# Optimization experiments

Measured on AMD Instinct MI355X. Metric: run time of the kernel, lower is better.

Reference implementation:

```python
import jax, jax.numpy as jnp
import numpy as np

B, N, D, H = 16, 256, 512, 8
DK = D // H          # 64
DIM_G = 64           # trigonometric geometry embedding dim
WAVE_LEN = 1000.0


def box_relational_embedding(boxes):
    # boxes: [B, N, 4] = (x_min, y_min, x_max, y_max)
    x_min, y_min, x_max, y_max = jnp.split(boxes, 4, axis=-1)  # each [B,N,1]
    cx = ((x_min + x_max) * 0.5)[..., 0]   # [B,N]
    cy = ((y_min + y_max) * 0.5)[..., 0]
    w = (x_max - x_min + 1.0)[..., 0]
    h = (y_max - y_min + 1.0)[..., 0]
    # pairwise deltas, normalized by the *row* box size (as in the torch code)
    dx = jnp.log(jnp.clip(jnp.abs((cx[:, :, None] - cx[:, None, :]) / w[:, :, None]), 1e-3))
    dy = jnp.log(jnp.clip(jnp.abs((cy[:, :, None] - cy[:, None, :]) / h[:, :, None]), 1e-3))
    dw = jnp.log(w[:, :, None] / w[:, None, :])
    dh = jnp.log(h[:, :, None] / h[:, None, :])
    pos = jnp.stack([dx, dy, dw, dh], axis=-1)  # [B,N,N,4]
    # trig embedding: freq per (dim_g/8) channels
    feat_range = jnp.arange(DIM_G // 8, dtype=pos.dtype) / (DIM_G / 8.0)
    dim_mat = 1.0 / jnp.power(WAVE_LEN, feat_range)               # [8]
    mul = (100.0 * pos)[..., None] * dim_mat                      # [B,N,N,4,8]
    mul = mul.reshape(mul.shape[:3] + (-1,))                      # [B,N,N,32]
    return jnp.concatenate([jnp.sin(mul), jnp.cos(mul)], axis=-1)  # [B,N,N,64]


def setup_inputs() -> dict:
    key = jax.random.key(0)
    ks = jax.random.split(key, 16)
    inp = {
        'input_query': jax.random.normal(ks[0], (B, N, D), jnp.float32),
        'input_key': jax.random.normal(ks[1], (B, N, D), jnp.float32),
        'input_value': jax.random.normal(ks[2], (B, N, D), jnp.float32),
    }
    # valid boxes: x_max > x_min, y_max > y_min
    xm = jax.random.uniform(ks[3], (B, N, 1)) * 800.0
    ym = jax.random.uniform(ks[4], (B, N, 1)) * 800.0
    bw = jax.random.uniform(ks[5], (B, N, 1)) * 120.0 + 5.0
    bh = jax.random.uniform(ks[6], (B, N, 1)) * 120.0 + 5.0
    inp['input_box'] = jnp.concatenate([xm, ym, xm + bw, ym + bh], axis=-1)
    s = 1.0 / np.sqrt(D)
    inp['Wq'] = jax.random.normal(ks[7], (D, D), jnp.float32) * s
    inp['bq'] = jnp.zeros((D,), jnp.float32)
    inp['Wk'] = jax.random.normal(ks[8], (D, D), jnp.float32) * s
    inp['bk'] = jnp.zeros((D,), jnp.float32)
    inp['Wv'] = jax.random.normal(ks[9], (D, D), jnp.float32) * s
    inp['bv'] = jnp.zeros((D,), jnp.float32)
    inp['Wo'] = jax.random.normal(ks[10], (D, D), jnp.float32) * s
    inp['bo'] = jnp.zeros((D,), jnp.float32)
    inp['Wg'] = jax.random.normal(ks[11], (H, DIM_G), jnp.float32) * (1.0 / np.sqrt(DIM_G))
    inp['bg'] = jnp.zeros((H,), jnp.float32)
    return inp


def reference(input_query, input_key, input_value, input_box,
              Wq, bq, Wk, bk, Wv, bv, Wo, bo, Wg, bg):
    nb = input_query.shape[0]
    geo = box_relational_embedding(input_box)                     # [B,N,N,64]
    wg = jax.nn.relu(jnp.einsum('bijg,hg->bhij', geo, Wg) + bg[None, :, None, None])
    def proj(x, W, b):
        return (x @ W + b).reshape(nb, -1, H, DK).transpose(0, 2, 1, 3)  # [B,H,N,dk]
    q = proj(input_query, Wq, bq)
    k = proj(input_key, Wk, bk)
    v = proj(input_value, Wv, bv)
    scores = jnp.einsum('bhid,bhjd->bhij', q, k) / np.sqrt(DK)    # [B,H,N,N]
    w_mn = jax.nn.softmax(jnp.log(jnp.clip(wg, 1e-6)) + scores, axis=-1)
    out = jnp.einsum('bhij,bhjd->bhid', w_mn, v)                  # [B,H,N,dk]
    out = out.transpose(0, 2, 1, 3).reshape(nb, -1, H * DK)       # [B,N,D]
    return out @ Wo + bo
```

## Files before the change

kernel.cpp:

```cpp
#include <hip/hip_runtime.h>
#include <hip/hip_bf16.h>

#define B_ 16
#define N_ 256
#define D_ 512
#define H_ 8
#define DK_ 64

typedef unsigned short u16;
typedef __attribute__((ext_vector_type(8))) short bf16x8;
typedef __attribute__((ext_vector_type(4))) float f32x4;

__device__ __forceinline__ float bf2f(u16 u) {
    union { unsigned int i; float f; } v;
    v.i = ((unsigned int)u) << 16;
    return v.f;
}
__device__ __forceinline__ u16 f2bf(float f) {
    union { float f; unsigned int i; } v;
    v.f = f;
    unsigned int x = v.i;
    unsigned int r = (x >> 16) & 1u;
    x += 0x7fffu + r;
    return (u16)(x >> 16);
}

__global__ __launch_bounds__(256) void k_prep(const float* __restrict__ box,
                                              const float* __restrict__ Wg,
                                              const float* __restrict__ bg,
                                              u16* __restrict__ Sg,
                                              const float* __restrict__ W0,
                                              const float* __restrict__ W1,
                                              const float* __restrict__ W2,
                                              const float* __restrict__ W3,
                                              u16* __restrict__ Wt,
                                              const float* __restrict__ X0,
                                              const float* __restrict__ X1,
                                              const float* __restrict__ X2,
                                              u16* __restrict__ Xb) {
    const int tid = threadIdx.x;
    const int bid = blockIdx.x;
    if (bid < 4096) {
        __shared__ float sWg[8][64];
        __shared__ float sbg[8];
        if (tid < 8) sbg[tid] = bg[tid];
        { int e = tid; sWg[e >> 6][e & 63] = Wg[e];
          e = tid + 256; sWg[e >> 6][e & 63] = Wg[e]; }
        const int bi = bid, b = bi >> 8;
        float4 bxi = *(const float4*)&box[(size_t)bi * 4];
        float4 bxj = *(const float4*)&box[(size_t)(b * N_ + tid) * 4];
        __syncthreads();
        float cxi = (bxi.x + bxi.z) * 0.5f, cyi = (bxi.y + bxi.w) * 0.5f;
        float wi = bxi.z - bxi.x + 1.0f, hi = bxi.w - bxi.y + 1.0f;
        float cxj = (bxj.x + bxj.z) * 0.5f, cyj = (bxj.y + bxj.w) * 0.5f;
        float wj = bxj.z - bxj.x + 1.0f, hj = bxj.w - bxj.y + 1.0f;
        float pos[4];
        pos[0] = __logf(fmaxf(fabsf((cxi - cxj) / wi), 1e-3f));
        pos[1] = __logf(fmaxf(fabsf((cyi - cyj) / hi), 1e-3f));
        pos[2] = __logf(wi / wj);
        pos[3] = __logf(hi / hj);
        const float dm[8] = {1.0f, 0.42169650342858224f, 0.1778279410038923f,
                             0.07498942093324559f, 0.03162277660168379f,
                             0.013335214321633241f, 0.005623413251903491f,
                             0.0023713737056616554f};
        const float inv2pi = 0.15915494309189535f;
        float acc[8];
#pragma unroll
        for (int h = 0; h < 8; ++h) acc[h] = sbg[h];
#pragma unroll
        for (int t = 0; t < 4; ++t) {
            float base = 100.0f * pos[t];
#pragma unroll
            for (int f = 0; f < 8; ++f) {
                float rev = base * dm[f] * inv2pi;
                rev = rev - floorf(rev);
                float sn = __builtin_amdgcn_sinf(rev);
                float cs = __builtin_amdgcn_cosf(rev);
                int idx = t * 8 + f;
#pragma unroll
                for (int h = 0; h < 8; ++h)
                    acc[h] += sWg[h][idx] * sn + sWg[h][idx + 32] * cs;
            }
        }
        const int i = bi & 255;
#pragma unroll
        for (int h = 0; h < 8; ++h)
            Sg[(((size_t)(b * H_ + h) * N_) + i) * N_ + tid] =
                f2bf(__logf(fmaxf(acc[h], 1e-6f)));
    } else if (bid < 5120) {
        __shared__ float tt[32][33];
        int t = bid - 4096;
        int z = t >> 8, yb = (t >> 4) & 15, xb = t & 15;
        const float* W = (z == 0) ? W0 : (z == 1) ? W1 : (z == 2) ? W2 : W3;
        u16* dst = Wt + (size_t)z * 262144;
        const int kb = yb * 32, nb = xb * 32;
#pragma unroll
        for (int r = 0; r < 4; ++r) {
            int p = r * 256 + tid;
            tt[p >> 5][p & 31] = W[(size_t)(kb + (p >> 5)) * 512 + nb + (p & 31)];
        }
        __syncthreads();
#pragma unroll
        for (int r = 0; r < 4; ++r) {
            int p = r * 256 + tid;
            dst[(size_t)(nb + (p >> 5)) * 512 + kb + (p & 31)] = f2bf(tt[p & 31][p >> 5]);
        }
    } else {
        int t = bid - 5120;
        int z = t >> 10, x = t & 1023;
        const float* X = (z == 0) ? X0 : (z == 1) ? X1 : X2;
        u16* dst = Xb + (size_t)z * 2097152;
        int base = (x * 256 + tid) * 8;
        float4 a = *(const float4*)&X[base];
        float4 b = *(const float4*)&X[base + 4];
        ushort4 oa, ob;
        oa.x = f2bf(a.x); oa.y = f2bf(a.y); oa.z = f2bf(a.z); oa.w = f2bf(a.w);
        ob.x = f2bf(b.x); ob.y = f2bf(b.y); ob.z = f2bf(b.z); ob.w = f2bf(b.w);
        *(ushort4*)&dst[base] = oa;
        *(ushort4*)&dst[base + 4] = ob;
    }
}

__global__ __launch_bounds__(256) void k_gemm_qkv(const u16* __restrict__ Xb,
                                                  const u16* __restrict__ Wtb,
                                                  const float* __restrict__ bq,
                                                  const float* __restrict__ bk,
                                                  const float* __restrict__ bv,
                                                  u16* __restrict__ qkv) {
    const int z = blockIdx.z;
    const u16* Ab = Xb + (size_t)z * 2097152;
    const u16* Wt = Wtb + (size_t)z * 262144;
    const float* bias = (z == 0) ? bq : (z == 1) ? bk : bv;
    u16* dst = qkv + (size_t)z * 2097152;

    __shared__ u16 As[2][64][72];
    __shared__ u16 Bs[2][64][72];
    const int tid = threadIdx.x;
    const int n0 = blockIdx.x * 64, m0 = blockIdx.y * 64;
    const int wid = tid >> 6, lane = tid & 63;
    const int wm = (wid & 1) * 32, wn = (wid >> 1) * 32;
    const int lr = lane & 15, lk8 = (lane >> 4) * 8, quad4 = (lane >> 4) * 4;

    f32x4 acc[2][2];
#pragma unroll
    for (int mi = 0; mi < 2; ++mi)
#pragma unroll
        for (int ni = 0; ni < 2; ++ni) acc[mi][ni] = (f32x4){0.f, 0.f, 0.f, 0.f};

    ushort4 ra[4], rb[4];
#pragma unroll
    for (int r = 0; r < 4; ++r) {
        int p = r * 256 + tid, row = p >> 4, c4 = (p & 15) * 4;
        ra[r] = *(const ushort4*)&Ab[(size_t)(m0 + row) * 512 + c4];
        rb[r] = *(const ushort4*)&Wt[(size_t)(n0 + row) * 512 + c4];
    }
#pragma unroll
    for (int r = 0; r < 4; ++r) {
        int p = r * 256 + tid, row = p >> 4, c4 = (p & 15) * 4;
        *(ushort4*)&As[0][row][c4] = ra[r];
        *(ushort4*)&Bs[0][row][c4] = rb[r];
    }
    __syncthreads();
    for (int it = 0; it < 8; ++it) {
        const int cur = it & 1;
        if (it < 7) {
            int k0n = (it + 1) * 64;
#pragma unroll
            for (int r = 0; r < 4; ++r) {
                int p = r * 256 + tid, row = p >> 4, c4 = (p & 15) * 4;
                ra[r] = *(const ushort4*)&Ab[(size_t)(m0 + row) * 512 + k0n + c4];
                rb[r] = *(const ushort4*)&Wt[(size_t)(n0 + row) * 512 + k0n + c4];
            }
        }
#pragma unroll
        for (int ks = 0; ks < 64; ks += 32) {
            bf16x8 af[2], bfx[2];
#pragma unroll
            for (int mi = 0; mi < 2; ++mi)
                af[mi] = *(const bf16x8*)&As[cur][wm + mi * 16 + lr][ks + lk8];
#pragma unroll
            for (int ni = 0; ni < 2; ++ni)
                bfx[ni] = *(const bf16x8*)&Bs[cur][wn + ni * 16 + lr][ks + lk8];
#pragma unroll
            for (int mi = 0; mi < 2; ++mi)
#pragma unroll
                for (int ni = 0; ni < 2; ++ni)
                    acc[mi][ni] = __builtin_amdgcn_mfma_f32_16x16x32_bf16(
                        af[mi], bfx[ni], acc[mi][ni], 0, 0, 0);
        }
        if (it < 7) {
#pragma unroll
            for (int r = 0; r < 4; ++r) {
                int p = r * 256 + tid, row = p >> 4, c4 = (p & 15) * 4;
                *(ushort4*)&As[1 - cur][row][c4] = ra[r];
                *(ushort4*)&Bs[1 - cur][row][c4] = rb[r];
            }
            __syncthreads();
        }
    }
    u16* bounce = &As[0][0][0];
    const float scale = (z == 0) ? 0.125f : 1.0f;
    const int h = n0 >> 6, b = m0 >> 8, rrb = m0 & 255;
    if (z == 2) {
#pragma unroll
        for (int mi = 0; mi < 2; ++mi)
#pragma unroll
            for (int ni = 0; ni < 2; ++ni) {
                int cn = wn + ni * 16 + lr;
                float bb = bias[n0 + cn];
#pragma unroll
                for (int reg = 0; reg < 4; ++reg) {
                    int rm = wm + mi * 16 + quad4 + reg;
                    bounce[cn * 72 + rm] = f2bf(acc[mi][ni][reg] + bb);
                }
            }
        __syncthreads();
#pragma unroll
        for (int r = 0; r < 4; ++r) {
            int p = r * 256 + tid, dn = p >> 4, c4 = (p & 15) * 4;
            *(ushort4*)&dst[(((size_t)(b * H_ + h) * DK_) + dn) * N_ + rrb + c4] =
                *(const ushort4*)&bounce[dn * 72 + c4];
        }
    } else {
#pragma unroll
        for (int mi = 0; mi < 2; ++mi)
#pragma unroll
            for (int ni = 0; ni < 2; ++ni) {
                int cn = wn + ni * 16 + lr;
                float bb = bias[n0 + cn];
#pragma unroll
                for (int reg = 0; reg < 4; ++reg) {
                    int rm = wm + mi * 16 + quad4 + reg;
                    bounce[rm * 72 + cn] = f2bf((acc[mi][ni][reg] + bb) * scale);
                }
            }
        __syncthreads();
#pragma unroll
        for (int r = 0; r < 4; ++r) {
            int p = r * 256 + tid, rm = p >> 4, c4 = (p & 15) * 4;
            *(ushort4*)&dst[(((size_t)(b * H_ + h) * N_) + rrb + rm) * DK_ + c4] =
                *(const ushort4*)&bounce[rm * 72 + c4];
        }
    }
}

__global__ __launch_bounds__(256) void k_gemm_out(const u16* __restrict__ Ab,
                                                  const u16* __restrict__ Wt,
                                                  const float* __restrict__ bias,
                                                  float* __restrict__ outp) {
    __shared__ u16 As[2][64][72];
    __shared__ u16 Bs[2][64][72];
    const int tid = threadIdx.x;
    const int n0 = blockIdx.x * 64, m0 = blockIdx.y * 64;
    const int wid = tid >> 6, lane = tid & 63;
    const int wm = (wid & 1) * 32, wn = (wid >> 1) * 32;
    const int lr = lane & 15, lk8 = (lane >> 4) * 8;
    f32x4 acc[2][2];
#pragma unroll
    for (int mi = 0; mi < 2; ++mi)
#pragma unroll
        for (int ni = 0; ni < 2; ++ni) acc[mi][ni] = (f32x4){0.f, 0.f, 0.f, 0.f};
    ushort4 ra[4], rb[4];
#pragma unroll
    for (int r = 0; r < 4; ++r) {
        int p = r * 256 + tid, row = p >> 4, c4 = (p & 15) * 4;
        ra[r] = *(const ushort4*)&Ab[(size_t)(m0 + row) * 512 + c4];
        rb[r] = *(const ushort4*)&Wt[(size_t)(n0 + row) * 512 + c4];
    }
#pragma unroll
    for (int r = 0; r < 4; ++r) {
        int p = r * 256 + tid, row = p >> 4, c4 = (p & 15) * 4;
        *(ushort4*)&As[0][row][c4] = ra[r];
        *(ushort4*)&Bs[0][row][c4] = rb[r];
    }
    __syncthreads();
    for (int it = 0; it < 8; ++it) {
        const int cur = it & 1;
        if (it < 7) {
            int k0n = (it + 1) * 64;
#pragma unroll
            for (int r = 0; r < 4; ++r) {
                int p = r * 256 + tid, row = p >> 4, c4 = (p & 15) * 4;
                ra[r] = *(const ushort4*)&Ab[(size_t)(m0 + row) * 512 + k0n + c4];
                rb[r] = *(const ushort4*)&Wt[(size_t)(n0 + row) * 512 + k0n + c4];
            }
        }
#pragma unroll
        for (int ks = 0; ks < 64; ks += 32) {
            bf16x8 af[2], bfx[2];
#pragma unroll
            for (int mi = 0; mi < 2; ++mi)
                af[mi] = *(const bf16x8*)&As[cur][wm + mi * 16 + lr][ks + lk8];
#pragma unroll
            for (int ni = 0; ni < 2; ++ni)
                bfx[ni] = *(const bf16x8*)&Bs[cur][wn + ni * 16 + lr][ks + lk8];
#pragma unroll
            for (int mi = 0; mi < 2; ++mi)
#pragma unroll
                for (int ni = 0; ni < 2; ++ni)
                    acc[mi][ni] = __builtin_amdgcn_mfma_f32_16x16x32_bf16(
                        af[mi], bfx[ni], acc[mi][ni], 0, 0, 0);
        }
        if (it < 7) {
#pragma unroll
            for (int r = 0; r < 4; ++r) {
                int p = r * 256 + tid, row = p >> 4, c4 = (p & 15) * 4;
                *(ushort4*)&As[1 - cur][row][c4] = ra[r];
                *(ushort4*)&Bs[1 - cur][row][c4] = rb[r];
            }
            __syncthreads();
        }
    }
#pragma unroll
    for (int mi = 0; mi < 2; ++mi)
#pragma unroll
        for (int ni = 0; ni < 2; ++ni) {
            int col = n0 + wn + ni * 16 + lr;
            float bb = bias[col];
#pragma unroll
            for (int reg = 0; reg < 4; ++reg) {
                int m = m0 + wm + mi * 16 + (lane >> 4) * 4 + reg;
                outp[(size_t)m * 512 + col] = acc[mi][ni][reg] + bb;
            }
        }
}

__global__ __launch_bounds__(256) void k_attn(const u16* __restrict__ qh,
                                              const u16* __restrict__ kh,
                                              const u16* __restrict__ vhT,
                                              const u16* __restrict__ Sg,
                                              u16* __restrict__ attnb) {
    __shared__ __align__(16) unsigned char smem[40960];
    u16* sQ = (u16*)smem;
    u16* sP = (u16*)(smem + 4608);
    u16* sK = (u16*)(smem + 21504);
    u16* sVt = (u16*)(smem + 21504);
    float* sRedM = (float*)(smem + 39936);
    float* sRedS = (float*)(smem + 40448);

    const int tid = threadIdx.x;
    const int i0 = blockIdx.x * 32;
    const int bh = blockIdx.y;
    const int b = bh >> 3, h = bh & 7;
    const int wid = tid >> 6, lane = tid & 63;
    const int lr = lane & 15, lk8 = (lane >> 4) * 8, quad4 = (lane >> 4) * 4;

#pragma unroll
    for (int r = 0; r < 2; ++r) {
        int p = r * 256 + tid, i = p >> 4, d0 = (p & 15) * 4;
        *(ushort4*)&sQ[i * 72 + d0] =
            *(const ushort4*)&qh[((size_t)bh * N_ + i0 + i) * DK_ + d0];
    }
#pragma unroll
    for (int r = 0; r < 8; ++r) {
        int p = r * 256 + tid, row = p >> 6, jc = (p & 63) * 4;
        *(ushort4*)&sP[row * 264 + jc] =
            *(const ushort4*)&Sg[(((size_t)bh * N_) + i0 + row) * N_ + jc];
    }
#pragma unroll
    for (int r = 0; r < 8; ++r) {
        int p = r * 256 + tid, j = p >> 4, d0 = (p & 15) * 4;
        *(ushort4*)&sK[j * 72 + d0] =
            *(const ushort4*)&kh[((size_t)bh * N_ + j) * DK_ + d0];
    }
    __syncthreads();

    ushort4 kpre[8];
#pragma unroll
    for (int r = 0; r < 8; ++r) {
        int p = r * 256 + tid, j = p >> 4, d0 = (p & 15) * 4;
        kpre[r] = *(const ushort4*)&kh[((size_t)bh * N_ + 128 + j) * DK_ + d0];
    }
    f32x4 acc[2][2][2];
#pragma unroll
    for (int c = 0; c < 2; ++c)
#pragma unroll
        for (int mi = 0; mi < 2; ++mi)
#pragma unroll
            for (int ni = 0; ni < 2; ++ni) acc[c][mi][ni] = (f32x4){0.f, 0.f, 0.f, 0.f};
#pragma unroll
    for (int ks = 0; ks < 64; ks += 32) {
        bf16x8 af[2], bfx[2];
#pragma unroll
        for (int mi = 0; mi < 2; ++mi)
            af[mi] = *(const bf16x8*)&sQ[(mi * 16 + lr) * 72 + ks + lk8];
#pragma unroll
        for (int ni = 0; ni < 2; ++ni)
            bfx[ni] = *(const bf16x8*)&sK[(wid * 32 + ni * 16 + lr) * 72 + ks + lk8];
#pragma unroll
        for (int mi = 0; mi < 2; ++mi)
#pragma unroll
            for (int ni = 0; ni < 2; ++ni)
                acc[0][mi][ni] = __builtin_amdgcn_mfma_f32_16x16x32_bf16(
                    af[mi], bfx[ni], acc[0][mi][ni], 0, 0, 0);
    }
    __syncthreads();
#pragma unroll
    for (int r = 0; r < 8; ++r) {
        int p = r * 256 + tid, j = p >> 4, d0 = (p & 15) * 4;
        *(ushort4*)&sK[j * 72 + d0] = kpre[r];
    }
    __syncthreads();
#pragma unroll
    for (int ks = 0; ks < 64; ks += 32) {
        bf16x8 af[2], bfx[2];
#pragma unroll
        for (int mi = 0; mi < 2; ++mi)
            af[mi] = *(const bf16x8*)&sQ[(mi * 16 + lr) * 72 + ks + lk8];
#pragma unroll
        for (int ni = 0; ni < 2; ++ni)
            bfx[ni] = *(const bf16x8*)&sK[(wid * 32 + ni * 16 + lr) * 72 + ks + lk8];
#pragma unroll
        for (int mi = 0; mi < 2; ++mi)
#pragma unroll
            for (int ni = 0; ni < 2; ++ni)
                acc[1][mi][ni] = __builtin_amdgcn_mfma_f32_16x16x32_bf16(
                    af[mi], bfx[ni], acc[1][mi][ni], 0, 0, 0);
    }
    __syncthreads();

#pragma unroll
    for (int r = 0; r < 8; ++r) {
        int p = r * 256 + tid, d = p >> 5, jc = (p & 31) * 4;
        *(ushort4*)&sVt[d * 136 + jc] =
            *(const ushort4*)&vhT[(((size_t)bh * DK_) + d) * N_ + jc];
    }
#pragma unroll
    for (int c = 0; c < 2; ++c)
#pragma unroll
        for (int mi = 0; mi < 2; ++mi)
#pragma unroll
            for (int ni = 0; ni < 2; ++ni) {
                int col = c * 128 + wid * 32 + ni * 16 + lr;
#pragma unroll
                for (int reg = 0; reg < 4; ++reg) {
                    int row = mi * 16 + quad4 + reg;
                    acc[c][mi][ni][reg] += bf2f(sP[row * 264 + col]);
                }
            }
    float mrow[2][4];
#pragma unroll
    for (int mi = 0; mi < 2; ++mi)
#pragma unroll
        for (int reg = 0; reg < 4; ++reg) {
            float m = acc[0][mi][0][reg];
            m = fmaxf(m, acc[0][mi][1][reg]);
            m = fmaxf(m, acc[1][mi][0][reg]);
            m = fmaxf(m, acc[1][mi][1][reg]);
#pragma unroll
            for (int off = 1; off <= 8; off <<= 1) m = fmaxf(m, __shfl_xor(m, off, 64));
            mrow[mi][reg] = m;
        }
    if (lr == 0) {
#pragma unroll
        for (int mi = 0; mi < 2; ++mi)
#pragma unroll
            for (int reg = 0; reg < 4; ++reg)
                sRedM[(mi * 16 + quad4 + reg) * 4 + wid] = mrow[mi][reg];
    }
    __syncthreads();
    float gm[2][4], sl[2][4];
#pragma unroll
    for (int mi = 0; mi < 2; ++mi)
#pragma unroll
        for (int reg = 0; reg < 4; ++reg) {
            float4 mm = *(const float4*)&sRedM[(mi * 16 + quad4 + reg) * 4];
            gm[mi][reg] = fmaxf(fmaxf(mm.x, mm.y), fmaxf(mm.z, mm.w));
            sl[mi][reg] = 0.f;
        }
#pragma unroll
    for (int c = 0; c < 2; ++c)
#pragma unroll
        for (int mi = 0; mi < 2; ++mi)
#pragma unroll
            for (int ni = 0; ni < 2; ++ni)
#pragma unroll
                for (int reg = 0; reg < 4; ++reg) {
                    float e = __expf(acc[c][mi][ni][reg] - gm[mi][reg]);
                    acc[c][mi][ni][reg] = e;
                    sl[mi][reg] += e;
                }
#pragma unroll
    for (int mi = 0; mi < 2; ++mi)
#pragma unroll
        for (int reg = 0; reg < 4; ++reg) {
            float s = sl[mi][reg];
#pragma unroll
            for (int off = 1; off <= 8; off <<= 1) s += __shfl_xor(s, off, 64);
            sl[mi][reg] = s;
        }
    if (lr == 0) {
#pragma unroll
        for (int mi = 0; mi < 2; ++mi)
#pragma unroll
            for (int reg = 0; reg < 4; ++reg)
                sRedS[(mi * 16 + quad4 + reg) * 4 + wid] = sl[mi][reg];
    }
    __syncthreads();
#pragma unroll
    for (int mi = 0; mi < 2; ++mi)
#pragma unroll
        for (int reg = 0; reg < 4; ++reg) {
            float4 ss = *(const float4*)&sRedS[(mi * 16 + quad4 + reg) * 4];
            gm[mi][reg] = 1.0f / (ss.x + ss.y + ss.z + ss.w);
        }
#pragma unroll
    for (int c = 0; c < 2; ++c)
#pragma unroll
        for (int mi = 0; mi < 2; ++mi)
#pragma unroll
            for (int ni = 0; ni < 2; ++ni) {
                int col = c * 128 + wid * 32 + ni * 16 + lr;
#pragma unroll
                for (int reg = 0; reg < 4; ++reg) {
                    int row = mi * 16 + quad4 + reg;
                    sP[row * 264 + col] = f2bf(acc[c][mi][ni][reg] * gm[mi][reg]);
                }
            }
    __syncthreads();

    f32x4 o[2];
    o[0] = (f32x4){0.f, 0.f, 0.f, 0.f};
    o[1] = (f32x4){0.f, 0.f, 0.f, 0.f};
#pragma unroll
    for (int k0 = 0; k0 < 128; k0 += 32) {
        bf16x8 bfx = *(const bf16x8*)&sVt[(wid * 16 + lr) * 136 + k0 + lk8];
#pragma unroll
        for (int mi = 0; mi < 2; ++mi) {
            bf16x8 af = *(const bf16x8*)&sP[(mi * 16 + lr) * 264 + k0 + lk8];
            o[mi] = __builtin_amdgcn_mfma_f32_16x16x32_bf16(af, bfx, o[mi], 0, 0, 0);
        }
    }
    __syncthreads();
#pragma unroll
    for (int r = 0; r < 8; ++r) {
        int p = r * 256 + tid, d = p >> 5, jc = (p & 31) * 4;
        *(ushort4*)&sVt[d * 136 + jc] =
            *(const ushort4*)&vhT[(((size_t)bh * DK_) + d) * N_ + 128 + jc];
    }
    __syncthreads();
#pragma unroll
    for (int k0 = 0; k0 < 128; k0 += 32) {
        bf16x8 bfx = *(const bf16x8*)&sVt[(wid * 16 + lr) * 136 + k0 + lk8];
#pragma unroll
        for (int mi = 0; mi < 2; ++mi) {
            bf16x8 af = *(const bf16x8*)&sP[(mi * 16 + lr) * 264 + 128 + k0 + lk8];
            o[mi] = __builtin_amdgcn_mfma_f32_16x16x32_bf16(af, bfx, o[mi], 0, 0, 0);
        }
    }
#pragma unroll
    for (int mi = 0; mi < 2; ++mi)
#pragma unroll
        for (int reg = 0; reg < 4; ++reg) {
            int row = mi * 16 + quad4 + reg;
            attnb[((size_t)(b * N_ + i0 + row)) * D_ + h * 64 + wid * 16 + lr] =
                f2bf(o[mi][reg]);
        }
}

extern "C" void kernel_launch(void* const* d_in, const int* in_sizes, int n_in,
                              void* d_out, int out_size, void* d_ws, size_t ws_size,
                              hipStream_t stream) {
    const float* Xq = (const float*)d_in[0];
    const float* Xk = (const float*)d_in[1];
    const float* Xv = (const float*)d_in[2];
    const float* box = (const float*)d_in[3];
    const float* Wq = (const float*)d_in[4];
    const float* bq = (const float*)d_in[5];
    const float* Wk = (const float*)d_in[6];
    const float* bk = (const float*)d_in[7];
    const float* Wv = (const float*)d_in[8];
    const float* bv = (const float*)d_in[9];
    const float* Wo = (const float*)d_in[10];
    const float* bo = (const float*)d_in[11];
    const float* Wg = (const float*)d_in[12];
    const float* bg = (const float*)d_in[13];
    float* out = (float*)d_out;

    u16* ws16 = (u16*)d_ws;
    u16* qkv = ws16;
    u16* qh = qkv;
    u16* kh = qkv + 2097152;
    u16* vhT = qkv + 4194304;
    u16* Sg = ws16 + 6291456;
    u16* attnb = ws16 + 14680064;
    u16* Wt = ws16 + 16777216;
    u16* Xb = ws16 + 18874368;

    dim3 blk(256);
    k_prep<<<dim3(8192), blk, 0, stream>>>(box, Wg, bg, Sg, Wq, Wk, Wv, Wo, Wt,
                                           Xq, Xk, Xv, Xb);
    k_gemm_qkv<<<dim3(8, 64, 3), blk, 0, stream>>>(Xb, Wt, bq, bk, bv, qkv);
    k_attn<<<dim3(8, 128), blk, 0, stream>>>(qh, kh, vhT, Sg, attnb);
    k_gemm_out<<<dim3(8, 64), blk, 0, stream>>>(attnb, Wt + 3 * 262144, bo, out);
}
```

Measured before the change: 169.4 us.

## Move geometry bias computation into the QKV GEMM launch to overlap work

The trig-heavy geometric bias computation (4096 blocks) moves out of the prep kernel and into the QKV projection kernel as extra blocks. The QKV GEMM's 1536 MFMA blocks and the ALU-bound geometry blocks then share one grid and can co-schedule on the CUs. The prep kernel keeps only the weight transpose and input bf16 conversion. Shared memory becomes a single union buffer, and the larger LDS footprint applies to the geometry blocks as well, which may lower their occupancy.

```diff
diff --git a/kernel.cpp b/kernel.cpp
--- a/kernel.cpp
+++ b/kernel.cpp
@@ -25,28 +25,187 @@
     return (u16)(x >> 16);
 }
 
-__global__ __launch_bounds__(256) void k_prep(const float* __restrict__ box,
-                                              const float* __restrict__ Wg,
-                                              const float* __restrict__ bg,
-                                              u16* __restrict__ Sg,
-                                              const float* __restrict__ W0,
-                                              const float* __restrict__ W1,
-                                              const float* __restrict__ W2,
-                                              const float* __restrict__ W3,
-                                              u16* __restrict__ Wt,
-                                              const float* __restrict__ X0,
-                                              const float* __restrict__ X1,
-                                              const float* __restrict__ X2,
-                                              u16* __restrict__ Xb) {
+__global__ __launch_bounds__(256) void k_prep_lite(const float* __restrict__ W0,
+                                                   const float* __restrict__ W1,
+                                                   const float* __restrict__ W2,
+                                                   const float* __restrict__ W3,
+                                                   u16* __restrict__ Wt,
+                                                   const float* __restrict__ X0,
+                                                   const float* __restrict__ X1,
+                                                   const float* __restrict__ X2,
+                                                   u16* __restrict__ Xb) {
     const int tid = threadIdx.x;
     const int bid = blockIdx.x;
-    if (bid < 4096) {
-        __shared__ float sWg[8][64];
-        __shared__ float sbg[8];
+    if (bid < 1024) {
+        __shared__ float tt[32][33];
+        int t = bid;
+        int z = t >> 8, yb = (t >> 4) & 15, xb = t & 15;
+        const float* W = (z == 0) ? W0 : (z == 1) ? W1 : (z == 2) ? W2 : W3;
+        u16* dst = Wt + (size_t)z * 262144;
+        const int kb = yb * 32, nb = xb * 32;
+#pragma unroll
+        for (int r = 0; r < 4; ++r) {
+            int p = r * 256 + tid;
+            tt[p >> 5][p & 31] = W[(size_t)(kb + (p >> 5)) * 512 + nb + (p & 31)];
+        }
+        __syncthreads();
+#pragma unroll
+        for (int r = 0; r < 4; ++r) {
+            int p = r * 256 + tid;
+            dst[(size_t)(nb + (p >> 5)) * 512 + kb + (p & 31)] = f2bf(tt[p & 31][p >> 5]);
+        }
+    } else {
+        int t = bid - 1024;
+        int z = t >> 10, x = t & 1023;
+        const float* X = (z == 0) ? X0 : (z == 1) ? X1 : X2;
+        u16* dst = Xb + (size_t)z * 2097152;
+        int base = (x * 256 + tid) * 8;
+        float4 a = *(const float4*)&X[base];
+        float4 b = *(const float4*)&X[base + 4];
+        ushort4 oa, ob;
+        oa.x = f2bf(a.x); oa.y = f2bf(a.y); oa.z = f2bf(a.z); oa.w = f2bf(a.w);
+        ob.x = f2bf(b.x); ob.y = f2bf(b.y); ob.z = f2bf(b.z); ob.w = f2bf(b.w);
+        *(ushort4*)&dst[base] = oa;
+        *(ushort4*)&dst[base + 4] = ob;
+    }
+}
+
+__global__ __launch_bounds__(256) void k_qkv_geo(const u16* __restrict__ Xb,
+                                                 const u16* __restrict__ Wtb,
+                                                 const float* __restrict__ bq,
+                                                 const float* __restrict__ bk,
+                                                 const float* __restrict__ bv,
+                                                 u16* __restrict__ qkv,
+                                                 const float* __restrict__ box,
+                                                 const float* __restrict__ Wg,
+                                                 const float* __restrict__ bg,
+                                                 u16* __restrict__ Sg) {
+    __shared__ __align__(16) unsigned char smem[36864];
+    const int tid = threadIdx.x;
+    const int bid = blockIdx.x;
+    if (bid < 1536) {
+        u16* As = (u16*)smem;
+        u16* Bs = (u16*)(smem + 18432);
+        const int z = bid >> 9, t = bid & 511;
+        const int n0 = (t & 7) * 64, m0 = (t >> 3) * 64;
+        const u16* Ab = Xb + (size_t)z * 2097152;
+        const u16* Wt = Wtb + (size_t)z * 262144;
+        const float* bias = (z == 0) ? bq : (z == 1) ? bk : bv;
+        u16* dst = qkv + (size_t)z * 2097152;
+        const int wid = tid >> 6, lane = tid & 63;
+        const int wm = (wid & 1) * 32, wn = (wid >> 1) * 32;
+        const int lr = lane & 15, lk8 = (lane >> 4) * 8, quad4 = (lane >> 4) * 4;
+
+        f32x4 acc[2][2];
+#pragma unroll
+        for (int mi = 0; mi < 2; ++mi)
+#pragma unroll
+            for (int ni = 0; ni < 2; ++ni) acc[mi][ni] = (f32x4){0.f, 0.f, 0.f, 0.f};
+
+        ushort4 ra[4], rb[4];
+#pragma unroll
+        for (int r = 0; r < 4; ++r) {
+            int p = r * 256 + tid, row = p >> 4, c4 = (p & 15) * 4;
+            ra[r] = *(const ushort4*)&Ab[(size_t)(m0 + row) * 512 + c4];
+            rb[r] = *(const ushort4*)&Wt[(size_t)(n0 + row) * 512 + c4];
+        }
+#pragma unroll
+        for (int r = 0; r < 4; ++r) {
+            int p = r * 256 + tid, row = p >> 4, c4 = (p & 15) * 4;
+            *(ushort4*)&As[(0 * 64 + row) * 72 + c4] = ra[r];
+            *(ushort4*)&Bs[(0 * 64 + row) * 72 + c4] = rb[r];
+        }
+        __syncthreads();
+        for (int it = 0; it < 8; ++it) {
+            const int cur = it & 1;
+            if (it < 7) {
+                int k0n = (it + 1) * 64;
+#pragma unroll
+                for (int r = 0; r < 4; ++r) {
+                    int p = r * 256 + tid, row = p >> 4, c4 = (p & 15) * 4;
+                    ra[r] = *(const ushort4*)&Ab[(size_t)(m0 + row) * 512 + k0n + c4];
+                    rb[r] = *(const ushort4*)&Wt[(size_t)(n0 + row) * 512 + k0n + c4];
+                }
+            }
+#pragma unroll
+            for (int ks = 0; ks < 64; ks += 32) {
+                bf16x8 af[2], bfx[2];
+#pragma unroll
+                for (int mi = 0; mi < 2; ++mi)
+                    af[mi] = *(const bf16x8*)&As[(cur * 64 + wm + mi * 16 + lr) * 72 + ks + lk8];
+#pragma unroll
+                for (int ni = 0; ni < 2; ++ni)
+                    bfx[ni] = *(const bf16x8*)&Bs[(cur * 64 + wn + ni * 16 + lr) * 72 + ks + lk8];
+#pragma unroll
+                for (int mi = 0; mi < 2; ++mi)
+#pragma unroll
+                    for (int ni = 0; ni < 2; ++ni)
+                        acc[mi][ni] = __builtin_amdgcn_mfma_f32_16x16x32_bf16(
+                            af[mi], bfx[ni], acc[mi][ni], 0, 0, 0);
+            }
+            if (it < 7) {
+                const int nxt = 1 - cur;
+#pragma unroll
+                for (int r = 0; r < 4; ++r) {
+                    int p = r * 256 + tid, row = p >> 4, c4 = (p & 15) * 4;
+                    *(ushort4*)&As[(nxt * 64 + row) * 72 + c4] = ra[r];
+                    *(ushort4*)&Bs[(nxt * 64 + row) * 72 + c4] = rb[r];
+                }
+                __syncthreads();
+            }
+        }
+        u16* bounce = (u16*)smem;
+        const float scale = (z == 0) ? 0.125f : 1.0f;
+        const int h = n0 >> 6, b = m0 >> 8, rrb = m0 & 255;
+        __syncthreads();
+        if (z == 2) {
+#pragma unroll
+            for (int mi = 0; mi < 2; ++mi)
+#pragma unroll
+                for (int ni = 0; ni < 2; ++ni) {
+                    int cn = wn + ni * 16 + lr;
+                    float bb = bias[n0 + cn];
+#pragma unroll
+                    for (int reg = 0; reg < 4; ++reg) {
+                        int rm = wm + mi * 16 + quad4 + reg;
+                        bounce[cn * 72 + rm] = f2bf(acc[mi][ni][reg] + bb);
+                    }
+                }
+            __syncthreads();
+#pragma unroll
+            for (int r = 0; r < 4; ++r) {
+                int p = r * 256 + tid, dn = p >> 4, c4 = (p & 15) * 4;
+                *(ushort4*)&dst[(((size_t)(b * H_ + h) * DK_) + dn) * N_ + rrb + c4] =
+                    *(const ushort4*)&bounce[dn * 72 + c4];
+            }
+        } else {
+#pragma unroll
+            for (int mi = 0; mi < 2; ++mi)
+#pragma unroll
+                for (int ni = 0; ni < 2; ++ni) {
+                    int cn = wn + ni * 16 + lr;
+                    float bb = bias[n0 + cn];
+#pragma unroll
+                    for (int reg = 0; reg < 4; ++reg) {
+                        int rm = wm + mi * 16 + quad4 + reg;
+                        bounce[rm * 72 + cn] = f2bf((acc[mi][ni][reg] + bb) * scale);
+                    }
+                }
+            __syncthreads();
+#pragma unroll
+            for (int r = 0; r < 4; ++r) {
+                int p = r * 256 + tid, rm = p >> 4, c4 = (p & 15) * 4;
+                *(ushort4*)&dst[(((size_t)(b * H_ + h) * N_) + rrb + rm) * DK_ + c4] =
+                    *(const ushort4*)&bounce[rm * 72 + c4];
+            }
+        }
+    } else {
+        float* sWg = (float*)smem;
+        float* sbg = (float*)(smem + 2048);
         if (tid < 8) sbg[tid] = bg[tid];
-        { int e = tid; sWg[e >> 6][e & 63] = Wg[e];
-          e = tid + 256; sWg[e >> 6][e & 63] = Wg[e]; }
-        const int bi = bid, b = bi >> 8;
+        { int e = tid; sWg[(e >> 6) * 64 + (e & 63)] = Wg[e];
+          e = tid + 256; sWg[(e >> 6) * 64 + (e & 63)] = Wg[e]; }
+        const int bi = bid - 1536, b = bi >> 8;
         float4 bxi = *(const float4*)&box[(size_t)bi * 4];
         float4 bxj = *(const float4*)&box[(size_t)(b * N_ + tid) * 4];
         __syncthreads();
@@ -79,7 +238,7 @@
                 int idx = t * 8 + f;
 #pragma unroll
                 for (int h = 0; h < 8; ++h)
-                    acc[h] += sWg[h][idx] * sn + sWg[h][idx + 32] * cs;
+                    acc[h] += sWg[h * 64 + idx] * sn + sWg[h * 64 + idx + 32] * cs;
             }
         }
         const int i = bi & 255;
@@ -87,160 +246,6 @@
         for (int h = 0; h < 8; ++h)
             Sg[(((size_t)(b * H_ + h) * N_) + i) * N_ + tid] =
                 f2bf(__logf(fmaxf(acc[h], 1e-6f)));
-    } else if (bid < 5120) {
-        __shared__ float tt[32][33];
-        int t = bid - 4096;
-        int z = t >> 8, yb = (t >> 4) & 15, xb = t & 15;
-        const float* W = (z == 0) ? W0 : (z == 1) ? W1 : (z == 2) ? W2 : W3;
-        u16* dst = Wt + (size_t)z * 262144;
-        const int kb = yb * 32, nb = xb * 32;
-#pragma unroll
-        for (int r = 0; r < 4; ++r) {
-            int p = r * 256 + tid;
-            tt[p >> 5][p & 31] = W[(size_t)(kb + (p >> 5)) * 512 + nb + (p & 31)];
-        }
-        __syncthreads();
-#pragma unroll
-        for (int r = 0; r < 4; ++r) {
-            int p = r * 256 + tid;
-            dst[(size_t)(nb + (p >> 5)) * 512 + kb + (p & 31)] = f2bf(tt[p & 31][p >> 5]);
-        }
-    } else {
-        int t = bid - 5120;
-        int z = t >> 10, x = t & 1023;
-        const float* X = (z == 0) ? X0 : (z == 1) ? X1 : X2;
-        u16* dst = Xb + (size_t)z * 2097152;
-        int base = (x * 256 + tid) * 8;
-        float4 a = *(const float4*)&X[base];
-        float4 b = *(const float4*)&X[base + 4];
-        ushort4 oa, ob;
-        oa.x = f2bf(a.x); oa.y = f2bf(a.y); oa.z = f2bf(a.z); oa.w = f2bf(a.w);
-        ob.x = f2bf(b.x); ob.y = f2bf(b.y); ob.z = f2bf(b.z); ob.w = f2bf(b.w);
-        *(ushort4*)&dst[base] = oa;
-        *(ushort4*)&dst[base + 4] = ob;
-    }
-}
-
-__global__ __launch_bounds__(256) void k_gemm_qkv(const u16* __restrict__ Xb,
-                                                  const u16* __restrict__ Wtb,
-                                                  const float* __restrict__ bq,
-                                                  const float* __restrict__ bk,
-                                                  const float* __restrict__ bv,
-                                                  u16* __restrict__ qkv) {
-    const int z = blockIdx.z;
-    const u16* Ab = Xb + (size_t)z * 2097152;
-    const u16* Wt = Wtb + (size_t)z * 262144;
-    const float* bias = (z == 0) ? bq : (z == 1) ? bk : bv;
-    u16* dst = qkv + (size_t)z * 2097152;
-
-    __shared__ u16 As[2][64][72];
-    __shared__ u16 Bs[2][64][72];
-    const int tid = threadIdx.x;
-    const int n0 = blockIdx.x * 64, m0 = blockIdx.y * 64;
-    const int wid = tid >> 6, lane = tid & 63;
-    const int wm = (wid & 1) * 32, wn = (wid >> 1) * 32;
-    const int lr = lane & 15, lk8 = (lane >> 4) * 8, quad4 = (lane >> 4) * 4;
-
-    f32x4 acc[2][2];
-#pragma unroll
-    for (int mi = 0; mi < 2; ++mi)
-#pragma unroll
-        for (int ni = 0; ni < 2; ++ni) acc[mi][ni] = (f32x4){0.f, 0.f, 0.f, 0.f};
-
-    ushort4 ra[4], rb[4];
-#pragma unroll
-    for (int r = 0; r < 4; ++r) {
-        int p = r * 256 + tid, row = p >> 4, c4 = (p & 15) * 4;
-        ra[r] = *(const ushort4*)&Ab[(size_t)(m0 + row) * 512 + c4];
-        rb[r] = *(const ushort4*)&Wt[(size_t)(n0 + row) * 512 + c4];
-    }
-#pragma unroll
-    for (int r = 0; r < 4; ++r) {
-        int p = r * 256 + tid, row = p >> 4, c4 = (p & 15) * 4;
-        *(ushort4*)&As[0][row][c4] = ra[r];
-        *(ushort4*)&Bs[0][row][c4] = rb[r];
-    }
-    __syncthreads();
-    for (int it = 0; it < 8; ++it) {
-        const int cur = it & 1;
-        if (it < 7) {
-            int k0n = (it + 1) * 64;
-#pragma unroll
-            for (int r = 0; r < 4; ++r) {
-                int p = r * 256 + tid, row = p >> 4, c4 = (p & 15) * 4;
-                ra[r] = *(const ushort4*)&Ab[(size_t)(m0 + row) * 512 + k0n + c4];
-                rb[r] = *(const ushort4*)&Wt[(size_t)(n0 + row) * 512 + k0n + c4];
-            }
-        }
-#pragma unroll
-        for (int ks = 0; ks < 64; ks += 32) {
-            bf16x8 af[2], bfx[2];
-#pragma unroll
-            for (int mi = 0; mi < 2; ++mi)
-                af[mi] = *(const bf16x8*)&As[cur][wm + mi * 16 + lr][ks + lk8];
-#pragma unroll
-            for (int ni = 0; ni < 2; ++ni)
-                bfx[ni] = *(const bf16x8*)&Bs[cur][wn + ni * 16 + lr][ks + lk8];
-#pragma unroll
-            for (int mi = 0; mi < 2; ++mi)
-#pragma unroll
-                for (int ni = 0; ni < 2; ++ni)
-                    acc[mi][ni] = __builtin_amdgcn_mfma_f32_16x16x32_bf16(
-                        af[mi], bfx[ni], acc[mi][ni], 0, 0, 0);
-        }
-        if (it < 7) {
-#pragma unroll
-            for (int r = 0; r < 4; ++r) {
-                int p = r * 256 + tid, row = p >> 4, c4 = (p & 15) * 4;
-                *(ushort4*)&As[1 - cur][row][c4] = ra[r];
-                *(ushort4*)&Bs[1 - cur][row][c4] = rb[r];
-            }
-            __syncthreads();
-        }
-    }
-    u16* bounce = &As[0][0][0];
-    const float scale = (z == 0) ? 0.125f : 1.0f;
-    const int h = n0 >> 6, b = m0 >> 8, rrb = m0 & 255;
-    if (z == 2) {
-#pragma unroll
-        for (int mi = 0; mi < 2; ++mi)
-#pragma unroll
-            for (int ni = 0; ni < 2; ++ni) {
-                int cn = wn + ni * 16 + lr;
-                float bb = bias[n0 + cn];
-#pragma unroll
-                for (int reg = 0; reg < 4; ++reg) {
-                    int rm = wm + mi * 16 + quad4 + reg;
-                    bounce[cn * 72 + rm] = f2bf(acc[mi][ni][reg] + bb);
-                }
-            }
-        __syncthreads();
-#pragma unroll
-        for (int r = 0; r < 4; ++r) {
-            int p = r * 256 + tid, dn = p >> 4, c4 = (p & 15) * 4;
-            *(ushort4*)&dst[(((size_t)(b * H_ + h) * DK_) + dn) * N_ + rrb + c4] =
-                *(const ushort4*)&bounce[dn * 72 + c4];
-        }
-    } else {
-#pragma unroll
-        for (int mi = 0; mi < 2; ++mi)
-#pragma unroll
-            for (int ni = 0; ni < 2; ++ni) {
-                int cn = wn + ni * 16 + lr;
-                float bb = bias[n0 + cn];
-#pragma unroll
-                for (int reg = 0; reg < 4; ++reg) {
-                    int rm = wm + mi * 16 + quad4 + reg;
-                    bounce[rm * 72 + cn] = f2bf((acc[mi][ni][reg] + bb) * scale);
-                }
-            }
-        __syncthreads();
-#pragma unroll
-        for (int r = 0; r < 4; ++r) {
-            int p = r * 256 + tid, rm = p >> 4, c4 = (p & 15) * 4;
-            *(ushort4*)&dst[(((size_t)(b * H_ + h) * N_) + rrb + rm) * DK_ + c4] =
-                *(const ushort4*)&bounce[rm * 72 + c4];
-        }
     }
 }
 
@@ -588,9 +593,9 @@
     u16* Xb = ws16 + 18874368;
 
     dim3 blk(256);
-    k_prep<<<dim3(8192), blk, 0, stream>>>(box, Wg, bg, Sg, Wq, Wk, Wv, Wo, Wt,
-                                           Xq, Xk, Xv, Xb);
-    k_gemm_qkv<<<dim3(8, 64, 3), blk, 0, stream>>>(Xb, Wt, bq, bk, bv, qkv);
+    k_prep_lite<<<dim3(4096), blk, 0, stream>>>(Wq, Wk, Wv, Wo, Wt, Xq, Xk, Xv, Xb);
+    k_qkv_geo<<<dim3(5632), blk, 0, stream>>>(Xb, Wt, bq, bk, bv, qkv,
+                                              box, Wg, bg, Sg);
     k_attn<<<dim3(8, 128), blk, 0, stream>>>(qh, kh, vhT, Sg, attnb);
-    k_gemm_out<<<dim3(8, 64), blk, 0, stream>>>(attnb, Wt + 3 * 262144, bo, out);
+    k_gemm_out<<<dim3(8, 64), blk, 0, stream>>>(attnb, Wo == nullptr ? nullptr : Wt + 3 * 262144, bo, out);
 }
```

New measurement: 171.7 us. Within noise of the previous version (+1.4%).
